# Performance work log

Hardware: AMD Instinct MI355X
Metric: run time of the kernel (lower is better)

## Reference

```python
import jax, jax.numpy as jnp
import numpy as np

B, T, E, H, DH = 8, 1024, 1024, 16, 64

def setup_inputs() -> dict:
    key = jax.random.key(0)
    ks = jax.random.split(key, 5)
    x = jax.random.normal(ks[0], (B, T, E), dtype=jnp.float32)
    Wq = jax.random.normal(ks[1], (H, E, DH), dtype=jnp.float32) * (E ** -0.5)
    Wk = jax.random.normal(ks[2], (H, E, DH), dtype=jnp.float32) * (E ** -0.5)
    Wv = jax.random.normal(ks[3], (H, E, DH), dtype=jnp.float32) * (E ** -0.5)
    Wp = jax.random.normal(ks[4], (E, E), dtype=jnp.float32) * (E ** -0.5)
    bp = jnp.zeros((E,), dtype=jnp.float32)
    return {"x": x, "Wq": Wq, "Wk": Wk, "Wv": Wv, "Wp": Wp, "bp": bp}

def reference(x, Wq, Wk, Wv, Wp, bp):
    # per-head projections (bias-free), vectorized over heads
    q = jnp.einsum('bte,hed->bhtd', x, Wq)
    k = jnp.einsum('bte,hed->bhtd', x, Wk)
    v = jnp.einsum('bte,hed->bhtd', x, Wv)
    scale = DH ** -0.5
    att = jnp.einsum('bhtd,bhsd->bhts', q, k) * scale  # [B,H,T,T]
    causal = jnp.tril(jnp.ones((T, T), dtype=bool))
    att = jnp.where(causal, att, -jnp.inf)
    att = jax.nn.softmax(att, axis=-1)
    # dropout is identity in eval mode
    out = jnp.einsum('bhts,bhsd->bhtd', att, v)
    out = out.transpose(0, 2, 1, 3).reshape(B, T, E)  # concat heads in order
    # proj: torch Linear y = x @ W^T + b
    out = out @ Wp.T + bp
    return out
```

## Files before the change

### kernel.cpp

```cpp
#include <hip/hip_runtime.h>

#define Bsz 8
#define Tsz 1024
#define Esz 1024
#define Hsz 16
#define DHsz 64

typedef _Float16 f16x8 __attribute__((ext_vector_type(8)));
typedef float f32x4 __attribute__((ext_vector_type(4)));
typedef unsigned short u16x8 __attribute__((ext_vector_type(8)));

__device__ __forceinline__ unsigned short f2h(float f) {
    union { _Float16 h; unsigned short u; } cv;
    cv.h = (_Float16)f;
    return cv.u;
}

__device__ __forceinline__ void async16(const void* g, void* l) {
    __builtin_amdgcn_global_load_lds(
        (const __attribute__((address_space(1))) void*)g,
        (__attribute__((address_space(3))) void*)l, 16, 0, 0);
}

#define MFMA(a, b, c) __builtin_amdgcn_mfma_f32_16x16x32_f16((a), (b), (c), 0, 0, 0)


__global__ void cast_f16_kernel(const float* __restrict__ in, unsigned short* __restrict__ outp) {
    int i = (blockIdx.x * 256 + threadIdx.x) * 4;
    float4 v = *(const float4*)(in + i);
    ushort4 o;
    o.x = f2h(v.x); o.y = f2h(v.y); o.z = f2h(v.z); o.w = f2h(v.w);
    *(ushort4*)(outp + i) = o;
}

__global__ void pack_wqkv_kernel(const float* __restrict__ Wq, const float* __restrict__ Wk,
                                 const float* __restrict__ Wv, unsigned short* __restrict__ Bt) {
    int i = (blockIdx.x * 256 + threadIdx.x) * 4;
    int n = i >> 10;
    int e = i & 1023;
    int which = n >> 10, rem = n & 1023, h = rem >> 6, d = rem & 63;
    const float* W = (which == 0) ? Wq : ((which == 1) ? Wk : Wv);
    const float* src = W + ((size_t)h * Esz + e) * DHsz + d;
    ushort4 o;
    o.x = f2h(src[0]);
    o.y = f2h(src[DHsz]);
    o.z = f2h(src[2 * DHsz]);
    o.w = f2h(src[3 * DHsz]);
    *(ushort4*)(Bt + i) = o;
}

__global__ __launch_bounds__(256) void vtrans_kernel(const unsigned short* __restrict__ V,
                                                     unsigned short* __restrict__ VT) {
    __shared__ unsigned int tile[64 * 33];
    const int bh = blockIdx.x, tc = blockIdx.y;
    const int tid = threadIdx.x;
    const unsigned short* src = V + ((size_t)bh * Tsz + tc * 64) * DHsz;
#pragma unroll
    for (int it = 0; it < 2; ++it) {
        int task = tid + it * 256;
        int row = task >> 3, seg = task & 7;
        u16x8 v = *(const u16x8*)(src + row * DHsz + seg * 8);
#pragma unroll
        for (int jj = 0; jj < 4; ++jj)
            tile[row * 33 + seg * 4 + jj] =
                (unsigned int)v[2 * jj] | ((unsigned int)v[2 * jj + 1] << 16);
    }
    __syncthreads();
    unsigned short* dst = VT + (size_t)bh * DHsz * Tsz + tc * 64;
#pragma unroll
    for (int it = 0; it < 2; ++it) {
        int task = tid + it * 256;
        int d = task & 63, tseg = task >> 6;
        int du = d >> 1, hi = d & 1;
        u16x8 v;
#pragma unroll
        for (int j = 0; j < 8; ++j) {
            unsigned int w = tile[(tseg * 8 + j) * 33 + du];
            v[j] = (unsigned short)(hi ? (w >> 16) : (w & 0xffffu));
        }
        *(u16x8*)(dst + (size_t)d * Tsz + tseg * 8) = v;
    }
}

template <int MODE>
__global__ __launch_bounds__(256, 2) void gemm_bt(
    const unsigned short* __restrict__ A,
    const unsigned short* __restrict__ Bt,
    int K, int N,
    unsigned short* __restrict__ qo, unsigned short* __restrict__ ko,
    unsigned short* __restrict__ vo,
    float* __restrict__ outp, const float* __restrict__ bias)
{
    __shared__ unsigned short sA[128 * 32];
    __shared__ unsigned short sB[128 * 32];
    const int tid = threadIdx.x;
    const int wid = tid >> 6, lane = tid & 63;
    const int quad = lane >> 4, l16 = lane & 15;
    const int col0 = blockIdx.x * 128;
    const int row0 = blockIdx.y * 128;
    const int wm = (wid >> 1) * 64, wn = (wid & 1) * 64;

    const f32x4 zero4 = {0.f, 0.f, 0.f, 0.f};
    f32x4 acc[4][4];
#pragma unroll
    for (int i = 0; i < 4; ++i)
#pragma unroll
        for (int j = 0; j < 4; ++j) acc[i][j] = zero4;

    const unsigned short* gA = A + (size_t)row0 * K;
    const unsigned short* gB = Bt + (size_t)col0 * K;
    const int c0 = wid * 2;
    const int srw = lane >> 2;
    const int ssg = (lane & 3) * 8;

    for (int k0 = 0; k0 < K; k0 += 32) {
#pragma unroll
        for (int cc = 0; cc < 2; ++cc) {
            int c = c0 + cc;
            async16(gA + (size_t)(c * 16 + srw) * K + k0 + ssg, (void*)(sA + c * 512 + lane * 8));
            async16(gB + (size_t)(c * 16 + srw) * K + k0 + ssg, (void*)(sB + c * 512 + lane * 8));
        }
        __syncthreads();

        f16x8 af[4], bfr[4];
#pragma unroll
        for (int i = 0; i < 4; ++i)
            af[i] = *(const f16x8*)(sA + (wm + i * 16 + l16) * 32 + quad * 8);
#pragma unroll
        for (int j = 0; j < 4; ++j)
            bfr[j] = *(const f16x8*)(sB + (wn + j * 16 + l16) * 32 + quad * 8);
#pragma unroll
        for (int i = 0; i < 4; ++i)
#pragma unroll
            for (int j = 0; j < 4; ++j)
                acc[i][j] = MFMA(af[i], bfr[j], acc[i][j]);
        __syncthreads();
    }

    if (MODE == 0) {
#pragma unroll
        for (int j = 0; j < 4; ++j) {
            int c = col0 + wn + j * 16 + l16;
            int which = c >> 10, rem = c & 1023, h = rem >> 6, d = rem & 63;
            unsigned short* dst = (which == 0) ? qo : ((which == 1) ? ko : vo);
#pragma unroll
            for (int i = 0; i < 4; ++i) {
                int rb = row0 + wm + i * 16 + quad * 4;
#pragma unroll
                for (int r = 0; r < 4; ++r) {
                    int row = rb + r;
                    int b = row >> 10, t = row & 1023;
                    dst[((size_t)(b * Hsz + h) * Tsz + t) * DHsz + d] = f2h(acc[i][j][r]);
                }
            }
        }
    } else {
#pragma unroll
        for (int i = 0; i < 4; ++i) {
            int rb = row0 + wm + i * 16 + quad * 4;
#pragma unroll
            for (int r = 0; r < 4; ++r) {
                float* orow = outp + (size_t)(rb + r) * N;
#pragma unroll
                for (int j = 0; j < 4; ++j) {
                    int c = col0 + wn + j * 16 + l16;
                    orow[c] = acc[i][j][r] + bias[c];
                }
            }
        }
    }
}

__global__ __launch_bounds__(256, 3) void attn_kernel(
    const unsigned short* __restrict__ Q,
    const unsigned short* __restrict__ Kg,
    const unsigned short* __restrict__ VTg,
    unsigned short* __restrict__ AO)
{
    const int bh = blockIdx.x;
    const int pair = blockIdx.y;
    const int b = bh >> 4, h = bh & 15;
    const int tid = threadIdx.x, wid = tid >> 6, lane = tid & 63;
    const int quad = lane >> 4, l16 = lane & 15;

    __shared__ unsigned short sK[64 * 64];
    __shared__ unsigned short sVt[64 * 64];
    __shared__ unsigned short sP[128 * 72];

    const unsigned short* Qb = Q + (size_t)bh * Tsz * DHsz;
    const unsigned short* Kb = Kg + (size_t)bh * Tsz * DHsz;
    const unsigned short* VTb = VTg + (size_t)bh * DHsz * Tsz;

    const int srow = lane >> 3;
    const int sseg = lane & 7;
    const int slog = sseg ^ srow;

    const float C1 = 0.18033688f;
    const float C2 = -4.32808512f;
    const f32x4 zero4 = {0.f, 0.f, 0.f, 0.f};

    for (int half = 0; half < 2; ++half) {
        const int qt = (half == 0) ? (7 - pair) : pair;
        const int q0 = qt * 128;
        const int rowlo = q0 + wid * 32;
        const int prow0 = wid * 32;

        f16x8 qf[2][2];
#pragma unroll
        for (int rt = 0; rt < 2; ++rt)
#pragma unroll
            for (int kk = 0; kk < 2; ++kk)
                qf[rt][kk] = *(const f16x8*)(Qb + (size_t)(rowlo + rt * 16 + l16) * DHsz +
                                             kk * 32 + quad * 8);

        f32x4 o[2][4];
        float lp[2][4];
#pragma unroll
        for (int rt = 0; rt < 2; ++rt) {
#pragma unroll
            for (int dt = 0; dt < 4; ++dt) o[rt][dt] = zero4;
#pragma unroll
            for (int r = 0; r < 4; ++r) lp[rt][r] = 0.f;
        }

        const int nblk = (q0 >> 6) + 2;
        for (int blk = 0; blk < nblk; ++blk) {
            const int s0 = blk * 64;
            __syncthreads();
            {
                const int r0 = wid * 16;
#pragma unroll
                for (int ii = 0; ii < 2; ++ii) {
                    int rr = r0 + ii * 8;
                    async16(Kb + (size_t)(s0 + rr + srow) * DHsz + slog * 8,
                            (void*)(sK + rr * 64 + lane * 8));
                    async16(VTb + (size_t)(rr + srow) * Tsz + s0 + slog * 8,
                            (void*)(sVt + rr * 64 + lane * 8));
                }
            }
            __syncthreads();

            if (s0 > rowlo + 31) continue;

            f32x4 sc[2][4];
#pragma unroll
            for (int rt = 0; rt < 2; ++rt)
#pragma unroll
                for (int ct = 0; ct < 4; ++ct) sc[rt][ct] = zero4;
#pragma unroll
            for (int kk = 0; kk < 2; ++kk) {
                f16x8 kf[4];
#pragma unroll
                for (int ct = 0; ct < 4; ++ct)
                    kf[ct] = *(const f16x8*)(sK + (ct * 16 + l16) * 64 +
                                             (((kk * 4 + quad) ^ (l16 & 7)) * 8));
#pragma unroll
                for (int rt = 0; rt < 2; ++rt)
#pragma unroll
                    for (int ct = 0; ct < 4; ++ct)
                        sc[rt][ct] = MFMA(qf[rt][kk], kf[ct], sc[rt][ct]);
            }

            if (s0 + 63 <= rowlo) {
#pragma unroll
                for (int rt = 0; rt < 2; ++rt)
#pragma unroll
                    for (int r = 0; r < 4; ++r) {
                        unsigned short* pr = sP + (prow0 + rt * 16 + quad * 4 + r) * 72 + l16;
#pragma unroll
                        for (int ct = 0; ct < 4; ++ct) {
                            float p = exp2f(fmaf(sc[rt][ct][r], C1, C2));
                            lp[rt][r] += p;
                            pr[ct * 16] = f2h(p);
                        }
                    }
            } else {
#pragma unroll
                for (int rt = 0; rt < 2; ++rt)
#pragma unroll
                    for (int r = 0; r < 4; ++r) {
                        int qrow = rowlo + rt * 16 + quad * 4 + r;
                        unsigned short* pr = sP + (prow0 + rt * 16 + quad * 4 + r) * 72 + l16;
#pragma unroll
                        for (int ct = 0; ct < 4; ++ct) {
                            float p = exp2f(fmaf(sc[rt][ct][r], C1, C2));
                            p = (s0 + ct * 16 + l16 > qrow) ? 0.f : p;
                            lp[rt][r] += p;
                            pr[ct * 16] = f2h(p);
                        }
                    }
            }

#pragma unroll
            for (int kk = 0; kk < 2; ++kk) {
                f16x8 pf[2], vf[4];
#pragma unroll
                for (int rt = 0; rt < 2; ++rt)
                    pf[rt] = *(const f16x8*)(sP + (prow0 + rt * 16 + l16) * 72 +
                                             kk * 32 + quad * 8);
#pragma unroll
                for (int dt = 0; dt < 4; ++dt)
                    vf[dt] = *(const f16x8*)(sVt + (dt * 16 + l16) * 64 +
                                             (((kk * 4 + quad) ^ (l16 & 7)) * 8));
#pragma unroll
                for (int rt = 0; rt < 2; ++rt)
#pragma unroll
                    for (int dt = 0; dt < 4; ++dt)
                        o[rt][dt] = MFMA(pf[rt], vf[dt], o[rt][dt]);
            }
        }

#pragma unroll
        for (int rt = 0; rt < 2; ++rt)
#pragma unroll
            for (int r = 0; r < 4; ++r) {
                float s = lp[rt][r];
                s += __shfl_xor(s, 1, 64);
                s += __shfl_xor(s, 2, 64);
                s += __shfl_xor(s, 4, 64);
                s += __shfl_xor(s, 8, 64);
                float inv = 1.0f / s;
                int t = rowlo + rt * 16 + quad * 4 + r;
                size_t base = ((size_t)(b * Tsz + t)) * Esz + h * DHsz;
#pragma unroll
                for (int dt = 0; dt < 4; ++dt)
                    AO[base + dt * 16 + l16] = f2h(o[rt][dt][r] * inv);
            }
    }
}


extern "C" void kernel_launch(void* const* d_in, const int* in_sizes, int n_in,
                              void* d_out, int out_size, void* d_ws, size_t ws_size,
                              hipStream_t stream)
{
    const float* x  = (const float*)d_in[0];
    const float* Wq = (const float*)d_in[1];
    const float* Wk = (const float*)d_in[2];
    const float* Wv = (const float*)d_in[3];
    const float* Wp = (const float*)d_in[4];
    const float* bp = (const float*)d_in[5];
    float* out = (float*)d_out;

    char* ws = (char*)d_ws;
    unsigned short* xb   = (unsigned short*)(ws);
    unsigned short* wqkv = (unsigned short*)(ws + 16777216);
    unsigned short* wpb  = (unsigned short*)(ws + 23068672);
    unsigned short* qb   = (unsigned short*)(ws + 25165824);
    unsigned short* kb   = (unsigned short*)(ws + 41943040);
    unsigned short* vb   = (unsigned short*)(ws + 58720256);
    unsigned short* ao   = (unsigned short*)(ws + 75497472);
    unsigned short* vtb  = xb;

    cast_f16_kernel<<<8192, 256, 0, stream>>>(x, xb);
    pack_wqkv_kernel<<<3072, 256, 0, stream>>>(Wq, Wk, Wv, wqkv);
    cast_f16_kernel<<<1024, 256, 0, stream>>>(Wp, wpb);

    gemm_bt<0><<<dim3(24, 64), 256, 0, stream>>>(xb, wqkv, 1024, 3072,
                                                 qb, kb, vb, nullptr, nullptr);

    vtrans_kernel<<<dim3(128, 16), 256, 0, stream>>>(vb, vtb);

    attn_kernel<<<dim3(128, 4), 256, 0, stream>>>(qb, kb, vtb, ao);

    gemm_bt<1><<<dim3(8, 64), 256, 0, stream>>>(ao, wpb, 1024, 1024,
                                                nullptr, nullptr, nullptr, out, bp);
}
```

Before: 268.0 us.

## Store QKV as one row-major buffer via LDS-staged epilogue and split attention blocks

The QKV GEMM no longer scatters 2-byte stores into per-head Q/K/V tensors. It stages the tile in shared memory and writes coalesced 16-byte rows into a single [B*T, 3072] buffer. The attention and V-transpose kernels read Q, K and V from that buffer with a row stride of 3072. Attention now launches one block per query tile instead of pairing two tiles per block, and occupancy hints are raised for both kernels. The cost is strided rather than contiguous reads for Q and K in attention, plus less balanced per-block work in the causal launch.

```diff
diff --git a/kernel.cpp b/kernel.cpp
--- a/kernel.cpp
+++ b/kernel.cpp
@@ -5,6 +5,7 @@
 #define Esz 1024
 #define Hsz 16
 #define DHsz 64
+#define NQKV 3072
 
 typedef _Float16 f16x8 __attribute__((ext_vector_type(8)));
 typedef float f32x4 __attribute__((ext_vector_type(4)));
@@ -49,17 +50,18 @@
     *(ushort4*)(Bt + i) = o;
 }
 
-__global__ __launch_bounds__(256) void vtrans_kernel(const unsigned short* __restrict__ V,
+__global__ __launch_bounds__(256) void vtrans_kernel(const unsigned short* __restrict__ QKV,
                                                      unsigned short* __restrict__ VT) {
     __shared__ unsigned int tile[64 * 33];
     const int bh = blockIdx.x, tc = blockIdx.y;
+    const int b = bh >> 4, h = bh & 15;
     const int tid = threadIdx.x;
-    const unsigned short* src = V + ((size_t)bh * Tsz + tc * 64) * DHsz;
+    const unsigned short* src = QKV + ((size_t)(b * Tsz) + tc * 64) * NQKV + 2048 + h * 64;
 #pragma unroll
     for (int it = 0; it < 2; ++it) {
         int task = tid + it * 256;
         int row = task >> 3, seg = task & 7;
-        u16x8 v = *(const u16x8*)(src + row * DHsz + seg * 8);
+        u16x8 v = *(const u16x8*)(src + (size_t)row * NQKV + seg * 8);
 #pragma unroll
         for (int jj = 0; jj < 4; ++jj)
             tile[row * 33 + seg * 4 + jj] =
@@ -83,16 +85,16 @@
 }
 
 template <int MODE>
-__global__ __launch_bounds__(256, 2) void gemm_bt(
+__global__ __launch_bounds__(256, 3) void gemm_bt(
     const unsigned short* __restrict__ A,
     const unsigned short* __restrict__ Bt,
     int K, int N,
-    unsigned short* __restrict__ qo, unsigned short* __restrict__ ko,
-    unsigned short* __restrict__ vo,
+    unsigned short* __restrict__ c16,
     float* __restrict__ outp, const float* __restrict__ bias)
 {
-    __shared__ unsigned short sA[128 * 32];
-    __shared__ unsigned short sB[128 * 32];
+    __shared__ unsigned short smem[17408];
+    unsigned short* sA = smem;
+    unsigned short* sB = smem + 4096;
     const int tid = threadIdx.x;
     const int wid = tid >> 6, lane = tid & 63;
     const int quad = lane >> 4, l16 = lane & 15;
@@ -139,20 +141,22 @@
 
     if (MODE == 0) {
 #pragma unroll
-        for (int j = 0; j < 4; ++j) {
-            int c = col0 + wn + j * 16 + l16;
-            int which = c >> 10, rem = c & 1023, h = rem >> 6, d = rem & 63;
-            unsigned short* dst = (which == 0) ? qo : ((which == 1) ? ko : vo);
-#pragma unroll
-            for (int i = 0; i < 4; ++i) {
-                int rb = row0 + wm + i * 16 + quad * 4;
-#pragma unroll
-                for (int r = 0; r < 4; ++r) {
-                    int row = rb + r;
-                    int b = row >> 10, t = row & 1023;
-                    dst[((size_t)(b * Hsz + h) * Tsz + t) * DHsz + d] = f2h(acc[i][j][r]);
-                }
+        for (int i = 0; i < 4; ++i)
+#pragma unroll
+            for (int r = 0; r < 4; ++r) {
+                int rowL = wm + i * 16 + quad * 4 + r;
+                unsigned short* tr = smem + rowL * 136 + wn + l16;
+#pragma unroll
+                for (int j = 0; j < 4; ++j)
+                    tr[j * 16] = f2h(acc[i][j][r]);
             }
+        __syncthreads();
+        unsigned short* ob = c16 + (size_t)row0 * N + col0;
+#pragma unroll
+        for (int it = 0; it < 8; ++it) {
+            int rowG = wid * 32 + it * 4 + quad;
+            u16x8 v = *(const u16x8*)(smem + rowG * 136 + l16 * 8);
+            *(u16x8*)(ob + (size_t)rowG * N + l16 * 8) = v;
         }
     } else {
 #pragma unroll
@@ -171,15 +175,15 @@
     }
 }
 
-__global__ __launch_bounds__(256, 3) void attn_kernel(
-    const unsigned short* __restrict__ Q,
-    const unsigned short* __restrict__ Kg,
+__global__ __launch_bounds__(256, 4) void attn_kernel(
+    const unsigned short* __restrict__ QKV,
     const unsigned short* __restrict__ VTg,
     unsigned short* __restrict__ AO)
 {
     const int bh = blockIdx.x;
-    const int pair = blockIdx.y;
+    const int qt = 7 - blockIdx.y;
     const int b = bh >> 4, h = bh & 15;
+    const int q0 = qt * 128;
     const int tid = threadIdx.x, wid = tid >> 6, lane = tid & 63;
     const int quad = lane >> 4, l16 = lane & 15;
 
@@ -187,8 +191,8 @@
     __shared__ unsigned short sVt[64 * 64];
     __shared__ unsigned short sP[128 * 72];
 
-    const unsigned short* Qb = Q + (size_t)bh * Tsz * DHsz;
-    const unsigned short* Kb = Kg + (size_t)bh * Tsz * DHsz;
+    const unsigned short* Qb = QKV + (size_t)(b * Tsz) * NQKV + h * 64;
+    const unsigned short* Kb = QKV + (size_t)(b * Tsz) * NQKV + 1024 + h * 64;
     const unsigned short* VTb = VTg + (size_t)bh * DHsz * Tsz;
 
     const int srow = lane >> 3;
@@ -199,134 +203,130 @@
     const float C2 = -4.32808512f;
     const f32x4 zero4 = {0.f, 0.f, 0.f, 0.f};
 
-    for (int half = 0; half < 2; ++half) {
-        const int qt = (half == 0) ? (7 - pair) : pair;
-        const int q0 = qt * 128;
-        const int rowlo = q0 + wid * 32;
-        const int prow0 = wid * 32;
-
-        f16x8 qf[2][2];
+    const int rowlo = q0 + wid * 32;
+    const int prow0 = wid * 32;
+
+    f16x8 qf[2][2];
+#pragma unroll
+    for (int rt = 0; rt < 2; ++rt)
+#pragma unroll
+        for (int kk = 0; kk < 2; ++kk)
+            qf[rt][kk] = *(const f16x8*)(Qb + (size_t)(rowlo + rt * 16 + l16) * NQKV +
+                                         kk * 32 + quad * 8);
+
+    f32x4 o[2][4];
+    float lp[2][4];
+#pragma unroll
+    for (int rt = 0; rt < 2; ++rt) {
+#pragma unroll
+        for (int dt = 0; dt < 4; ++dt) o[rt][dt] = zero4;
+#pragma unroll
+        for (int r = 0; r < 4; ++r) lp[rt][r] = 0.f;
+    }
+
+    const int nblk = (q0 >> 6) + 2;
+    for (int blk = 0; blk < nblk; ++blk) {
+        const int s0 = blk * 64;
+        __syncthreads();
+        {
+            const int r0 = wid * 16;
+#pragma unroll
+            for (int ii = 0; ii < 2; ++ii) {
+                int rr = r0 + ii * 8;
+                async16(Kb + (size_t)(s0 + rr + srow) * NQKV + slog * 8,
+                        (void*)(sK + rr * 64 + lane * 8));
+                async16(VTb + (size_t)(rr + srow) * Tsz + s0 + slog * 8,
+                        (void*)(sVt + rr * 64 + lane * 8));
+            }
+        }
+        __syncthreads();
+
+        if (s0 > rowlo + 31) continue;
+
+        f32x4 sc[2][4];
 #pragma unroll
         for (int rt = 0; rt < 2; ++rt)
 #pragma unroll
-            for (int kk = 0; kk < 2; ++kk)
-                qf[rt][kk] = *(const f16x8*)(Qb + (size_t)(rowlo + rt * 16 + l16) * DHsz +
-                                             kk * 32 + quad * 8);
-
-        f32x4 o[2][4];
-        float lp[2][4];
-#pragma unroll
-        for (int rt = 0; rt < 2; ++rt) {
-#pragma unroll
-            for (int dt = 0; dt < 4; ++dt) o[rt][dt] = zero4;
-#pragma unroll
-            for (int r = 0; r < 4; ++r) lp[rt][r] = 0.f;
-        }
-
-        const int nblk = (q0 >> 6) + 2;
-        for (int blk = 0; blk < nblk; ++blk) {
-            const int s0 = blk * 64;
-            __syncthreads();
-            {
-                const int r0 = wid * 16;
-#pragma unroll
-                for (int ii = 0; ii < 2; ++ii) {
-                    int rr = r0 + ii * 8;
-                    async16(Kb + (size_t)(s0 + rr + srow) * DHsz + slog * 8,
-                            (void*)(sK + rr * 64 + lane * 8));
-                    async16(VTb + (size_t)(rr + srow) * Tsz + s0 + slog * 8,
-                            (void*)(sVt + rr * 64 + lane * 8));
+            for (int ct = 0; ct < 4; ++ct) sc[rt][ct] = zero4;
+#pragma unroll
+        for (int kk = 0; kk < 2; ++kk) {
+            f16x8 kf[4];
+#pragma unroll
+            for (int ct = 0; ct < 4; ++ct)
+                kf[ct] = *(const f16x8*)(sK + (ct * 16 + l16) * 64 +
+                                         (((kk * 4 + quad) ^ (l16 & 7)) * 8));
+#pragma unroll
+            for (int rt = 0; rt < 2; ++rt)
+#pragma unroll
+                for (int ct = 0; ct < 4; ++ct)
+                    sc[rt][ct] = MFMA(qf[rt][kk], kf[ct], sc[rt][ct]);
+        }
+
+        if (s0 + 63 <= rowlo) {
+#pragma unroll
+            for (int rt = 0; rt < 2; ++rt)
+#pragma unroll
+                for (int r = 0; r < 4; ++r) {
+                    unsigned short* pr = sP + (prow0 + rt * 16 + quad * 4 + r) * 72 + l16;
+#pragma unroll
+                    for (int ct = 0; ct < 4; ++ct) {
+                        float p = exp2f(fmaf(sc[rt][ct][r], C1, C2));
+                        lp[rt][r] += p;
+                        pr[ct * 16] = f2h(p);
+                    }
                 }
-            }
-            __syncthreads();
-
-            if (s0 > rowlo + 31) continue;
-
-            f32x4 sc[2][4];
-#pragma unroll
-            for (int rt = 0; rt < 2; ++rt)
-#pragma unroll
-                for (int ct = 0; ct < 4; ++ct) sc[rt][ct] = zero4;
-#pragma unroll
-            for (int kk = 0; kk < 2; ++kk) {
-                f16x8 kf[4];
-#pragma unroll
-                for (int ct = 0; ct < 4; ++ct)
-                    kf[ct] = *(const f16x8*)(sK + (ct * 16 + l16) * 64 +
-                                             (((kk * 4 + quad) ^ (l16 & 7)) * 8));
-#pragma unroll
-                for (int rt = 0; rt < 2; ++rt)
-#pragma unroll
-                    for (int ct = 0; ct < 4; ++ct)
-                        sc[rt][ct] = MFMA(qf[rt][kk], kf[ct], sc[rt][ct]);
-            }
-
-            if (s0 + 63 <= rowlo) {
-#pragma unroll
-                for (int rt = 0; rt < 2; ++rt)
-#pragma unroll
-                    for (int r = 0; r < 4; ++r) {
-                        unsigned short* pr = sP + (prow0 + rt * 16 + quad * 4 + r) * 72 + l16;
-#pragma unroll
-                        for (int ct = 0; ct < 4; ++ct) {
-                            float p = exp2f(fmaf(sc[rt][ct][r], C1, C2));
-                            lp[rt][r] += p;
-                            pr[ct * 16] = f2h(p);
-                        }
+        } else {
+#pragma unroll
+            for (int rt = 0; rt < 2; ++rt)
+#pragma unroll
+                for (int r = 0; r < 4; ++r) {
+                    int qrow = rowlo + rt * 16 + quad * 4 + r;
+                    unsigned short* pr = sP + (prow0 + rt * 16 + quad * 4 + r) * 72 + l16;
+#pragma unroll
+                    for (int ct = 0; ct < 4; ++ct) {
+                        float p = exp2f(fmaf(sc[rt][ct][r], C1, C2));
+                        p = (s0 + ct * 16 + l16 > qrow) ? 0.f : p;
+                        lp[rt][r] += p;
+                        pr[ct * 16] = f2h(p);
                     }
-            } else {
-#pragma unroll
-                for (int rt = 0; rt < 2; ++rt)
-#pragma unroll
-                    for (int r = 0; r < 4; ++r) {
-                        int qrow = rowlo + rt * 16 + quad * 4 + r;
-                        unsigned short* pr = sP + (prow0 + rt * 16 + quad * 4 + r) * 72 + l16;
-#pragma unroll
-                        for (int ct = 0; ct < 4; ++ct) {
-                            float p = exp2f(fmaf(sc[rt][ct][r], C1, C2));
-                            p = (s0 + ct * 16 + l16 > qrow) ? 0.f : p;
-                            lp[rt][r] += p;
-                            pr[ct * 16] = f2h(p);
-                        }
-                    }
-            }
-
-#pragma unroll
-            for (int kk = 0; kk < 2; ++kk) {
-                f16x8 pf[2], vf[4];
-#pragma unroll
-                for (int rt = 0; rt < 2; ++rt)
-                    pf[rt] = *(const f16x8*)(sP + (prow0 + rt * 16 + l16) * 72 +
-                                             kk * 32 + quad * 8);
+                }
+        }
+
+#pragma unroll
+        for (int kk = 0; kk < 2; ++kk) {
+            f16x8 pf[2], vf[4];
+#pragma unroll
+            for (int rt = 0; rt < 2; ++rt)
+                pf[rt] = *(const f16x8*)(sP + (prow0 + rt * 16 + l16) * 72 +
+                                         kk * 32 + quad * 8);
+#pragma unroll
+            for (int dt = 0; dt < 4; ++dt)
+                vf[dt] = *(const f16x8*)(sVt + (dt * 16 + l16) * 64 +
+                                         (((kk * 4 + quad) ^ (l16 & 7)) * 8));
+#pragma unroll
+            for (int rt = 0; rt < 2; ++rt)
 #pragma unroll
                 for (int dt = 0; dt < 4; ++dt)
-                    vf[dt] = *(const f16x8*)(sVt + (dt * 16 + l16) * 64 +
-                                             (((kk * 4 + quad) ^ (l16 & 7)) * 8));
-#pragma unroll
-                for (int rt = 0; rt < 2; ++rt)
-#pragma unroll
-                    for (int dt = 0; dt < 4; ++dt)
-                        o[rt][dt] = MFMA(pf[rt], vf[dt], o[rt][dt]);
-            }
-        }
-
-#pragma unroll
-        for (int rt = 0; rt < 2; ++rt)
-#pragma unroll
-            for (int r = 0; r < 4; ++r) {
-                float s = lp[rt][r];
-                s += __shfl_xor(s, 1, 64);
-                s += __shfl_xor(s, 2, 64);
-                s += __shfl_xor(s, 4, 64);
-                s += __shfl_xor(s, 8, 64);
-                float inv = 1.0f / s;
-                int t = rowlo + rt * 16 + quad * 4 + r;
-                size_t base = ((size_t)(b * Tsz + t)) * Esz + h * DHsz;
-#pragma unroll
-                for (int dt = 0; dt < 4; ++dt)
-                    AO[base + dt * 16 + l16] = f2h(o[rt][dt][r] * inv);
-            }
-    }
+                    o[rt][dt] = MFMA(pf[rt], vf[dt], o[rt][dt]);
+        }
+    }
+
+#pragma unroll
+    for (int rt = 0; rt < 2; ++rt)
+#pragma unroll
+        for (int r = 0; r < 4; ++r) {
+            float s = lp[rt][r];
+            s += __shfl_xor(s, 1, 64);
+            s += __shfl_xor(s, 2, 64);
+            s += __shfl_xor(s, 4, 64);
+            s += __shfl_xor(s, 8, 64);
+            float inv = 1.0f / s;
+            int t = rowlo + rt * 16 + quad * 4 + r;
+            size_t base = ((size_t)(b * Tsz + t)) * Esz + h * DHsz;
+#pragma unroll
+            for (int dt = 0; dt < 4; ++dt)
+                AO[base + dt * 16 + l16] = f2h(o[rt][dt][r] * inv);
+        }
 }
 
 
@@ -346,9 +346,7 @@
     unsigned short* xb   = (unsigned short*)(ws);
     unsigned short* wqkv = (unsigned short*)(ws + 16777216);
     unsigned short* wpb  = (unsigned short*)(ws + 23068672);
-    unsigned short* qb   = (unsigned short*)(ws + 25165824);
-    unsigned short* kb   = (unsigned short*)(ws + 41943040);
-    unsigned short* vb   = (unsigned short*)(ws + 58720256);
+    unsigned short* qkv  = (unsigned short*)(ws + 25165824);
     unsigned short* ao   = (unsigned short*)(ws + 75497472);
     unsigned short* vtb  = xb;
 
@@ -357,12 +355,12 @@
     cast_f16_kernel<<<1024, 256, 0, stream>>>(Wp, wpb);
 
     gemm_bt<0><<<dim3(24, 64), 256, 0, stream>>>(xb, wqkv, 1024, 3072,
-                                                 qb, kb, vb, nullptr, nullptr);
-
-    vtrans_kernel<<<dim3(128, 16), 256, 0, stream>>>(vb, vtb);
-
-    attn_kernel<<<dim3(128, 4), 256, 0, stream>>>(qb, kb, vtb, ao);
+                                                 qkv, nullptr, nullptr);
+
+    vtrans_kernel<<<dim3(128, 16), 256, 0, stream>>>(qkv, vtb);
+
+    attn_kernel<<<dim3(128, 8), 256, 0, stream>>>(qkv, vtb, ao);
 
     gemm_bt<1><<<dim3(8, 64), 256, 0, stream>>>(ao, wpb, 1024, 1024,
-                                                nullptr, nullptr, nullptr, out, bp);
-}
+                                                nullptr, out, bp);
+}
```

New measurement: 294.8 us. 10.0% more time.
